# Optimization experiments

Hardware: AMD Instinct MI355X
Metric: run time of the kernel (lower is better)

## Reference

```python
import jax, jax.numpy as jnp
import numpy as np

B, C, H, W = 16, 256, 32, 32
NH, DH = 16, 16          # n_heads, n_head_channels; NH*DH == C
STRIDE, KK = 2, 9        # offset conv stride / kernel (stage_idx=0)
Hk, Wk = 16, 16          # offset map size = H/stride
NS = Hk * Wk             # n_sample
EPS_LN, EPS_BN = 1e-5, 1e-5


def conv1x1(x, w, b=None):
    # x: [B,Ci,H,W], w: [Co,Ci]
    y = jnp.einsum('bihw,oi->bohw', x, w)
    if b is not None:
        y = y + b[None, :, None, None]
    return y


def dwconv(x, w, b):
    # depthwise conv, w: [C,1,KK,KK]
    y = jax.lax.conv_general_dilated(
        x, w, (STRIDE, STRIDE), [(KK // 2, KK // 2)] * 2,
        dimension_numbers=('NCHW', 'OIHW', 'NCHW'),
        feature_group_count=x.shape[1])
    return y + b[None, :, None, None]


def ln_channels(x, g, b):
    # LayerNormProxy: layer-norm over channel dim of NCHW
    m = jnp.mean(x, axis=1, keepdims=True)
    v = jnp.mean((x - m) ** 2, axis=1, keepdims=True)
    return (x - m) / jnp.sqrt(v + EPS_LN) * g[None, :, None, None] + b[None, :, None, None]


def ref_points(hk, wk, b):
    # normalized (y, x) reference grid in [-1, 1], matching _get_ref_points
    ry = (jnp.arange(hk, dtype=jnp.float32) + 0.5) / hk * 2.0 - 1.0
    rx = (jnp.arange(wk, dtype=jnp.float32) + 0.5) / wk * 2.0 - 1.0
    ref = jnp.stack(jnp.meshgrid(ry, rx, indexing='ij'), axis=-1)  # [hk,wk,2] (y,x)
    return jnp.broadcast_to(ref[None], (b, hk, wk, 2))


def grid_sample_bilinear(img, grid):
    # img: [B,C,H,W]; grid: [B,Hg,Wg,2] in (x,y) order, [-1,1], align_corners=True,
    # zeros padding (matches torch F.grid_sample defaults).
    Bi, Ci, Hi, Wi = img.shape
    gx = (grid[..., 0] + 1.0) * 0.5 * (Wi - 1)
    gy = (grid[..., 1] + 1.0) * 0.5 * (Hi - 1)
    x0 = jnp.floor(gx); y0 = jnp.floor(gy)
    x1 = x0 + 1.0;      y1 = y0 + 1.0
    wx1 = gx - x0; wx0 = 1.0 - wx1
    wy1 = gy - y0; wy0 = 1.0 - wy1
    imgf = img.reshape(Bi, Ci, Hi * Wi)

    def gather(yi, xi):
        valid = (yi >= 0) & (yi < Hi) & (xi >= 0) & (xi < Wi)
        idx = (jnp.clip(yi, 0, Hi - 1) * Wi + jnp.clip(xi, 0, Wi - 1)).astype(jnp.int32)
        v = jnp.take_along_axis(imgf, idx.reshape(Bi, 1, -1), axis=2)  # [B,C,Hg*Wg]
        return v * valid.reshape(Bi, 1, -1).astype(img.dtype)

    out = (gather(y0, x0) * (wy0 * wx0).reshape(Bi, 1, -1)
           + gather(y0, x1) * (wy0 * wx1).reshape(Bi, 1, -1)
           + gather(y1, x0) * (wy1 * wx0).reshape(Bi, 1, -1)
           + gather(y1, x1) * (wy1 * wx1).reshape(Bi, 1, -1))
    return out.reshape(Bi, Ci, grid.shape[1], grid.shape[2])


def setup_inputs() -> dict:
    key = jax.random.key(0)
    ks = jax.random.split(key, 16)
    s = 0.05
    return {
        'x':        jax.random.normal(ks[0], (B, C, H, W), jnp.float32),
        'wq':       jax.random.normal(ks[1], (C, C), jnp.float32) * s,
        'bq':       jax.random.normal(ks[2], (C,), jnp.float32) * s,
        'off_dw_w': jax.random.normal(ks[3], (C, 1, KK, KK), jnp.float32) * s,
        'off_dw_b': jax.random.normal(ks[4], (C,), jnp.float32) * s,
        'ln_g':     jnp.ones((C,), jnp.float32),
        'ln_b':     jnp.zeros((C,), jnp.float32),
        'off_pw_w': jax.random.normal(ks[5], (2, C), jnp.float32) * s,
        'wk':       jax.random.normal(ks[6], (C, C), jnp.float32) * s,
        'bk':       jax.random.normal(ks[7], (C,), jnp.float32) * s,
        'wv':       jax.random.normal(ks[8], (C, C), jnp.float32) * s,
        'bv':       jax.random.normal(ks[9], (C,), jnp.float32) * s,
        'wo':       jax.random.normal(ks[10], (C, C), jnp.float32) * s,
        'bo':       jax.random.normal(ks[11], (C,), jnp.float32) * s,
        'bn_g':     jnp.ones((C,), jnp.float32),
        'bn_b':     jnp.zeros((C,), jnp.float32),
        'bn_m':     jax.random.normal(ks[12], (C,), jnp.float32) * s,
        'bn_v':     jax.random.uniform(ks[13], (C,), jnp.float32) + 0.5,
    }


def reference(x, wq, bq, off_dw_w, off_dw_b, ln_g, ln_b, off_pw_w,
              wk, bk, wv, bv, wo, bo, bn_g, bn_b, bn_m, bn_v):
    q = conv1x1(x, wq, bq)                                 # [B,C,H,W]
    # offset branch (n_groups=1 so q_off == q)
    off = dwconv(q, off_dw_w, off_dw_b)                    # [B,C,Hk,Wk]
    off = jax.nn.gelu(ln_channels(off, ln_g, ln_b), approximate=False)
    offset = jnp.einsum('bihw,oi->bohw', off, off_pw_w)    # [B,2,Hk,Wk] (y,x)
    offset = jnp.transpose(offset, (0, 2, 3, 1))           # [B,Hk,Wk,2]
    ref = ref_points(Hk, Wk, B)
    pos = jnp.tanh(offset + ref)                           # offset_range_factor[0] < 0 branch
    # deformable sampling: grid takes (x,y)
    xs = grid_sample_bilinear(x, pos[..., ::-1])           # [B,C,Hk,Wk]
    xs = xs.reshape(B, C, 1, NS)
    k = conv1x1(xs, wk, bk).reshape(B * NH, DH, NS)
    v = conv1x1(xs, wv, bv).reshape(B * NH, DH, NS)
    qf = q.reshape(B * NH, DH, H * W)
    attn = jnp.einsum('bcm,bcn->bmn', qf, k) * (DH ** -0.5)  # [B*NH, H*W, NS]
    attn = jax.nn.softmax(attn, axis=2)
    out = jnp.einsum('bmn,bcn->bcm', attn, v).reshape(B, C, H, W)
    y = conv1x1(out, wo, bo)
    # BatchNorm2d in eval mode with running stats
    y = ((y - bn_m[None, :, None, None]) / jnp.sqrt(bn_v[None, :, None, None] + EPS_BN)
         * bn_g[None, :, None, None] + bn_b[None, :, None, None])
    return y
```

## Files before the change

kernel.cpp:

```cpp
#include <hip/hip_runtime.h>
#include <hip/hip_bf16.h>
#include <math.h>

#define BATCH 16
#define CH    256
#define HW    1024
#define NS    256
#define NH    16
#define DH    16

typedef __attribute__((ext_vector_type(8))) short short8v;
typedef __attribute__((ext_vector_type(4))) float float4v;

__device__ __forceinline__ unsigned short f2bf(float f) {
    union { float f; unsigned u; } v; v.f = f;
    unsigned r = v.u + 0x7FFFu + ((v.u >> 16) & 1u);
    return (unsigned short)(r >> 16);
}

__global__ __launch_bounds__(256) void prep_k(
    const float* __restrict__ wq, const float* __restrict__ wk,
    const float* __restrict__ wv, const float* __restrict__ wo,
    unsigned short* __restrict__ Wf,
    const float* __restrict__ x, unsigned short* __restrict__ xT)
{
    int blk = blockIdx.x;
    if (blk < 1024) {
        const float* W;
        switch (blk >> 8) {
            case 0: W = wq; break;
            case 1: W = wk; break;
            case 2: W = wv; break;
            default: W = wo; break;
        }
        int e = (blk & 255) * 256 + threadIdx.x;
        int i = e & 7, l = (e >> 3) & 63, kt = (e >> 9) & 7, ot = e >> 12;
        float v = W[(ot * 16 + (l & 15)) * 256 + kt * 32 + 8 * (l >> 4) + i];
        Wf[(blk >> 8) * 65536 + e] = f2bf(v);
    } else {
        int xb = blk - 1024;
        int b = xb >> 4, pblk = (xb >> 2) & 3, cblk = xb & 3;
        int p = pblk * 256 + threadIdx.x;
        const float* xp = x + (size_t)b * CH * HW + p;
        unsigned short* o = xT + ((size_t)b * HW + p) * CH;
        #pragma unroll
        for (int cc = 0; cc < 64; cc += 8) {
            int c0 = cblk * 64 + cc;
            short8v t;
            #pragma unroll
            for (int i = 0; i < 8; ++i) t[i] = (short)f2bf(xp[(size_t)(c0 + i) * HW]);
            *(short8v*)&o[c0] = t;
        }
    }
}

template<int P, int MODE>
__global__ __launch_bounds__(256) void gemm_k(
    const unsigned short* __restrict__ Wf, const unsigned short* __restrict__ XT,
    const float* __restrict__ bias,
    float* __restrict__ outF, unsigned short* __restrict__ outB,
    const float* __restrict__ bn_g, const float* __restrict__ bn_b,
    const float* __restrict__ bn_m, const float* __restrict__ bn_v)
{
    const int b = blockIdx.z;

    const int t = threadIdx.x, lane = t & 63, wvi = t >> 6;
    const int g = lane >> 4, col = lane & 15;
    const int o0 = blockIdx.x * 64;
    const int p0 = blockIdx.y * 128 + wvi * 32;
    const unsigned short* xb = XT + ((size_t)b * P + p0) * CH;

    float4v acc[4][2];
    #pragma unroll
    for (int mi = 0; mi < 4; ++mi)
        #pragma unroll
        for (int ni = 0; ni < 2; ++ni) {
            float4v z = {0.f, 0.f, 0.f, 0.f};
            acc[mi][ni] = z;
        }

    #pragma unroll
    for (int kt = 0; kt < 8; ++kt) {
        short8v af[4], bf[2];
        #pragma unroll
        for (int mi = 0; mi < 4; ++mi)
            af[mi] = *(const short8v*)&Wf[(((((o0 >> 4) + mi) * 8) + kt) * 64 + lane) * 8];
        #pragma unroll
        for (int ni = 0; ni < 2; ++ni)
            bf[ni] = *(const short8v*)&xb[(size_t)(ni * 16 + col) * CH + kt * 32 + 8 * g];
        #pragma unroll
        for (int mi = 0; mi < 4; ++mi)
            #pragma unroll
            for (int ni = 0; ni < 2; ++ni)
                acc[mi][ni] = __builtin_amdgcn_mfma_f32_16x16x32_bf16(
                    af[mi], bf[ni], acc[mi][ni], 0, 0, 0);
    }

    #pragma unroll
    for (int mi = 0; mi < 4; ++mi) {
        const int ob = o0 + mi * 16 + 4 * g;
        float bs[4];
        #pragma unroll
        for (int ii = 0; ii < 4; ++ii) bs[ii] = bias[ob + ii];

        if (MODE == 2) {
            float sc[4], sh[4];
            #pragma unroll
            for (int ii = 0; ii < 4; ++ii) {
                int o = ob + ii;
                float s = bn_g[o] * rsqrtf(bn_v[o] + 1e-5f);
                sc[ii] = s;
                sh[ii] = bn_b[o] - bn_m[o] * s + bs[ii] * s;
            }
            #pragma unroll
            for (int ni = 0; ni < 2; ++ni) {
                int p = p0 + ni * 16 + col;
                #pragma unroll
                for (int ii = 0; ii < 4; ++ii)
                    outF[((size_t)(b * CH + ob + ii)) * P + p] =
                        acc[mi][ni][ii] * sc[ii] + sh[ii];
            }
        } else {
            #pragma unroll
            for (int ni = 0; ni < 2; ++ni) {
                int p = p0 + ni * 16 + col;
                float v0 = acc[mi][ni][0] + bs[0];
                float v1 = acc[mi][ni][1] + bs[1];
                float v2 = acc[mi][ni][2] + bs[2];
                float v3 = acc[mi][ni][3] + bs[3];
                outF[((size_t)(b * CH + ob + 0)) * P + p] = v0;
                outF[((size_t)(b * CH + ob + 1)) * P + p] = v1;
                outF[((size_t)(b * CH + ob + 2)) * P + p] = v2;
                outF[((size_t)(b * CH + ob + 3)) * P + p] = v3;
                uint2 w;
                w.x = (unsigned)f2bf(v0) | ((unsigned)f2bf(v1) << 16);
                w.y = (unsigned)f2bf(v2) | ((unsigned)f2bf(v3) << 16);
                *(uint2*)&outB[((size_t)(b * P + p)) * CH + ob] = w;
            }
        }
    }
}

__global__ __launch_bounds__(256) void dwconv_k(
    const float* __restrict__ q, const float* __restrict__ w,
    const float* __restrict__ bias, float* __restrict__ off)
{
    int bc = blockIdx.x;
    int c  = bc & (CH - 1);
    __shared__ float plane[HW];
    __shared__ float kw[81];
    int t = threadIdx.x;
    const float* qp = q + (size_t)bc * HW;
    #pragma unroll
    for (int j = t; j < HW; j += 256) plane[j] = qp[j];
    if (t < 81) kw[t] = w[c * 81 + t];
    __syncthreads();
    int hk = t >> 4, wk = t & 15;
    float s = bias[c];
    int yb = hk * 2 - 4, xb = wk * 2 - 4;
    #pragma unroll
    for (int dy = 0; dy < 9; ++dy) {
        int yy = yb + dy;
        if ((unsigned)yy < 32u) {
            #pragma unroll
            for (int dx = 0; dx < 9; ++dx) {
                int xx = xb + dx;
                if ((unsigned)xx < 32u) s += kw[dy * 9 + dx] * plane[yy * 32 + xx];
            }
        }
    }
    off[(size_t)bc * NS + t] = s;
}

__device__ inline void block_reduce2(float& a, float& b, int t, float* sbuf)
{
    #pragma unroll
    for (int o = 32; o > 0; o >>= 1) {
        a += __shfl_down(a, o);
        b += __shfl_down(b, o);
    }
    int w = t >> 6;
    if ((t & 63) == 0) { sbuf[w * 2] = a; sbuf[w * 2 + 1] = b; }
    __syncthreads();
    a = sbuf[0] + sbuf[2] + sbuf[4] + sbuf[6];
    b = sbuf[1] + sbuf[3] + sbuf[5] + sbuf[7];
    __syncthreads();
}

__global__ __launch_bounds__(256) void lngs_k(
    const float* __restrict__ off, const float* __restrict__ ln_g,
    const float* __restrict__ ln_b, const float* __restrict__ pw,
    const float* __restrict__ x, unsigned short* __restrict__ xsT)
{
    __shared__ float sbuf[8];
    int bs = blockIdx.x;
    int b = bs >> 8, s = bs & 255;
    int c = threadIdx.x;
    float v = off[((size_t)(b * CH + c)) * NS + s];
    float a = v, q2 = v * v;
    block_reduce2(a, q2, c, sbuf);
    float mean = a * (1.0f / 256.0f);
    float var  = q2 * (1.0f / 256.0f) - mean * mean;
    float xn = (v - mean) * rsqrtf(var + 1e-5f) * ln_g[c] + ln_b[c];
    float g = 0.5f * xn * (1.0f + erff(xn * 0.70710678118654752f));
    float d0 = g * pw[c];
    float d1 = g * pw[CH + c];
    block_reduce2(d0, d1, c, sbuf);

    int hk = s >> 4, wk = s & 15;
    float ry = ((hk + 0.5f) / 16.0f) * 2.0f - 1.0f;
    float rx = ((wk + 0.5f) / 16.0f) * 2.0f - 1.0f;
    float py = tanhf(d0 + ry);
    float px = tanhf(d1 + rx);

    float gx = (px + 1.0f) * 0.5f * 31.0f;
    float gy = (py + 1.0f) * 0.5f * 31.0f;
    float x0f = floorf(gx), y0f = floorf(gy);
    int ix = (int)x0f, iy = (int)y0f;
    float wx1 = gx - x0f, wx0 = 1.0f - wx1;
    float wy1 = gy - y0f, wy0 = 1.0f - wy1;
    const float* img = x + ((size_t)b * CH + c) * HW;
    float v00 = ((unsigned)iy < 32u && (unsigned)ix < 32u) ? img[iy * 32 + ix] : 0.0f;
    float v01 = ((unsigned)iy < 32u && (unsigned)(ix + 1) < 32u) ? img[iy * 32 + ix + 1] : 0.0f;
    float v10 = ((unsigned)(iy + 1) < 32u && (unsigned)ix < 32u) ? img[(iy + 1) * 32 + ix] : 0.0f;
    float v11 = ((unsigned)(iy + 1) < 32u && (unsigned)(ix + 1) < 32u) ? img[(iy + 1) * 32 + ix + 1] : 0.0f;
    float vv = wy0 * wx0 * v00 + wy0 * wx1 * v01 + wy1 * wx0 * v10 + wy1 * wx1 * v11;
    xsT[(size_t)bs * CH + c] = f2bf(vv);
}

__global__ __launch_bounds__(256) void attn_fused_k(
    const unsigned short* __restrict__ qT, const unsigned short* __restrict__ xsT,
    const unsigned short* __restrict__ Wf,
    const float* __restrict__ bk, const float* __restrict__ bv,
    unsigned short* __restrict__ aoT)
{
    const int bh   = blockIdx.x >> 2;
    const int mseg = blockIdx.x & 3;
    const int b = bh >> 4, h = bh & 15;

    __shared__ short Kp[16 * 64 * 8];
    __shared__ short Vp[8 * 64 * 8];
    __shared__ short Ps[4][16 * 32];

    const int tid  = threadIdx.x;
    const int lane = tid & 63;
    const int wvi  = tid >> 6;
    const int col  = lane & 15;
    const int g    = lane >> 4;

    {
        const unsigned short* WfK = Wf + 1 * 65536 + h * 4096;
        const unsigned short* WfV = Wf + 2 * 65536 + h * 4096;
        float bk4[4];
        #pragma unroll
        for (int j = 0; j < 4; ++j) bk4[j] = bk[h * 16 + 4 * g + j];
        const float bvv = bv[h * 16 + col];

        #pragma unroll
        for (int tt = 0; tt < 4; ++tt) {
            const int t  = wvi * 4 + tt;
            const int n0 = t * 16;
            float4v accK = {0.f, 0.f, 0.f, 0.f};
            float4v accV = {0.f, 0.f, 0.f, 0.f};
            #pragma unroll
            for (int kt = 0; kt < 8; ++kt) {
                short8v xsf = *(const short8v*)&xsT[((size_t)(b * NS + n0 + col)) * CH + kt * 32 + 8 * g];
                short8v wkf = *(const short8v*)&WfK[(kt * 64 + lane) * 8];
                short8v wvf = *(const short8v*)&WfV[(kt * 64 + lane) * 8];
                accK = __builtin_amdgcn_mfma_f32_16x16x32_bf16(wkf, xsf, accK, 0, 0, 0);
                accV = __builtin_amdgcn_mfma_f32_16x16x32_bf16(xsf, wvf, accV, 0, 0, 0);
            }
            uint2 wrk;
            wrk.x = (unsigned)f2bf(accK[0] + bk4[0]) | ((unsigned)f2bf(accK[1] + bk4[1]) << 16);
            wrk.y = (unsigned)f2bf(accK[2] + bk4[2]) | ((unsigned)f2bf(accK[3] + bk4[3]) << 16);
            *(uint2*)&Kp[(t * 64 + (g >> 1) * 16 + col) * 8 + 4 * (g & 1)] = wrk;
            uint2 wrv;
            wrv.x = (unsigned)f2bf(accV[0] + bvv) | ((unsigned)f2bf(accV[1] + bvv) << 16);
            wrv.y = (unsigned)f2bf(accV[2] + bvv) | ((unsigned)f2bf(accV[3] + bvv) << 16);
            *(uint2*)&Vp[((t >> 1) * 64 + col + 16 * ((2 * t + (g >> 1)) & 3)) * 8 + 4 * (g & 1)] = wrv;
        }
        short8v z = {0, 0, 0, 0, 0, 0, 0, 0};
        #pragma unroll
        for (int e = tid; e < 512; e += 256) {
            int t = e >> 5, l = e & 31;
            *(short8v*)&Kp[(t * 64 + 32 + l) * 8] = z;
        }
    }
    __syncthreads();

    const unsigned short* Qb = qT + (size_t)b * HW * CH + h * 16;
    unsigned short*       Ob = aoT + (size_t)b * HW * CH + h * 16;
    char* pbase = (char*)Ps[wvi];

    for (int mt = 0; mt < 4; ++mt) {
        const int m0 = mseg * 256 + wvi * 64 + mt * 16;

        short8v qf = {0, 0, 0, 0, 0, 0, 0, 0};
        if (g < 2)
            qf = *(const short8v*)&Qb[(size_t)(m0 + col) * CH + 8 * g];

        float4v p[16];
        #pragma unroll
        for (int t = 0; t < 16; ++t) {
            short8v kf = *(const short8v*)&Kp[(t * 64 + lane) * 8];
            float4v z = {0.f, 0.f, 0.f, 0.f};
            p[t] = __builtin_amdgcn_mfma_f32_16x16x32_bf16(kf, qf, z, 0, 0, 0);
        }

        float mx = -1e30f;
        #pragma unroll
        for (int t = 0; t < 16; ++t)
            mx = fmaxf(mx, fmaxf(fmaxf(p[t][0], p[t][1]), fmaxf(p[t][2], p[t][3])));
        mx = fmaxf(mx, __shfl_xor(mx, 16));
        mx = fmaxf(mx, __shfl_xor(mx, 32));
        float sum = 0.f;
        #pragma unroll
        for (int t = 0; t < 16; ++t) {
            #pragma unroll
            for (int i = 0; i < 4; ++i) {
                float e = __expf((p[t][i] - mx) * 0.25f);
                p[t][i] = e;
                sum += e;
            }
        }
        sum += __shfl_xor(sum, 16);
        sum += __shfl_xor(sum, 32);
        const float inv = 1.0f / sum;

        float4v acc = {0.f, 0.f, 0.f, 0.f};
        #pragma unroll
        for (int c = 0; c < 8; ++c) {
            #pragma unroll
            for (int pp = 0; pp < 2; ++pp) {
                float4v pv = p[2 * c + pp];
                uint2 wr;
                wr.x = (unsigned)f2bf(pv[0]) | ((unsigned)f2bf(pv[1]) << 16);
                wr.y = (unsigned)f2bf(pv[2]) | ((unsigned)f2bf(pv[3]) << 16);
                *(uint2*)(pbase + ((col * 64 + (16 * pp + 4 * g) * 2) ^ ((col & 7) << 4))) = wr;
            }
            short8v pf = *(const short8v*)(pbase + ((col * 64 + 16 * g) ^ ((col & 7) << 4)));
            short8v vf = *(const short8v*)&Vp[(c * 64 + lane) * 8];
            acc = __builtin_amdgcn_mfma_f32_16x16x32_bf16(vf, pf, acc, 0, 0, 0);
        }

        uint2 w;
        w.x = (unsigned)f2bf(acc[0] * inv) | ((unsigned)f2bf(acc[1] * inv) << 16);
        w.y = (unsigned)f2bf(acc[2] * inv) | ((unsigned)f2bf(acc[3] * inv) << 16);
        *(uint2*)&Ob[(size_t)(m0 + col) * CH + 4 * g] = w;
    }
}

extern "C" void kernel_launch(void* const* d_in, const int* in_sizes, int n_in,
                              void* d_out, int out_size, void* d_ws, size_t ws_size,
                              hipStream_t stream)
{
    const float* x        = (const float*)d_in[0];
    const float* wq       = (const float*)d_in[1];
    const float* bq       = (const float*)d_in[2];
    const float* off_dw_w = (const float*)d_in[3];
    const float* off_dw_b = (const float*)d_in[4];
    const float* ln_g     = (const float*)d_in[5];
    const float* ln_b     = (const float*)d_in[6];
    const float* off_pw_w = (const float*)d_in[7];
    const float* wk       = (const float*)d_in[8];
    const float* bk       = (const float*)d_in[9];
    const float* wv       = (const float*)d_in[10];
    const float* bv       = (const float*)d_in[11];
    const float* wo       = (const float*)d_in[12];
    const float* bo       = (const float*)d_in[13];
    const float* bn_g     = (const float*)d_in[14];
    const float* bn_b     = (const float*)d_in[15];
    const float* bn_m     = (const float*)d_in[16];
    const float* bn_v     = (const float*)d_in[17];

    float* ws  = (float*)d_ws;
    float* q   = ws;
    float* off = q + 4194304;
    unsigned short* us  = (unsigned short*)(off + 1048576);
    unsigned short* Wf  = us;
    unsigned short* xT  = Wf  + 262144;
    unsigned short* qT  = xT  + 4194304;
    unsigned short* xsT = qT  + 4194304;
    unsigned short* aoT = xsT + 1048576;

    prep_k<<<1280, 256, 0, stream>>>(wq, wk, wv, wo, Wf, x, xT);
    gemm_k<HW, 0><<<dim3(4, 8, BATCH), 256, 0, stream>>>(
        Wf, xT, bq, q, qT, nullptr, nullptr, nullptr, nullptr);
    dwconv_k<<<BATCH * CH, 256, 0, stream>>>(q, off_dw_w, off_dw_b, off);
    lngs_k<<<BATCH * NS, 256, 0, stream>>>(off, ln_g, ln_b, off_pw_w, x, xsT);
    attn_fused_k<<<BATCH * NH * 4, 256, 0, stream>>>(qT, xsT, Wf, bk, bv, aoT);
    gemm_k<HW, 2><<<dim3(4, 8, BATCH), 256, 0, stream>>>(
        Wf + 3 * 65536, aoT, bo, (float*)d_out, nullptr,
        bn_g, bn_b, bn_m, bn_v);
}
```

Before: 121.9 us.

## Use one 1024-thread block per head to compute K/V once

The attention kernel now runs one 1024-thread block per (batch, head) instead of four 256-thread blocks. Each of the 16 waves projects one 16-sample K/V tile, so K/V are computed once per head rather than four times. K is stored compactly, with a single zero row shared by the upper lanes in place of zero padding. The 1/sqrt(dh) scale is folded into the bf16 copy of q, and the fp32 q stays unscaled for the offset path. The change also uses the built-in bf16 conversion and tree reductions for the softmax max and sum, at the cost of fewer, larger blocks (256 total), which may reduce occupancy.

```diff
diff --git a/kernel.cpp b/kernel.cpp
--- a/kernel.cpp
+++ b/kernel.cpp
@@ -13,9 +13,10 @@
 typedef __attribute__((ext_vector_type(4))) float float4v;
 
 __device__ __forceinline__ unsigned short f2bf(float f) {
-    union { float f; unsigned u; } v; v.f = f;
-    unsigned r = v.u + 0x7FFFu + ((v.u >> 16) & 1u);
-    return (unsigned short)(r >> 16);
+    return __builtin_bit_cast(unsigned short, __float2bfloat16(f));
+}
+__device__ __forceinline__ unsigned pack2(float lo, float hi) {
+    return (unsigned)f2bf(lo) | ((unsigned)f2bf(hi) << 16);
 }
 
 __global__ __launch_bounds__(256) void prep_k(
@@ -133,8 +134,8 @@
                 outF[((size_t)(b * CH + ob + 2)) * P + p] = v2;
                 outF[((size_t)(b * CH + ob + 3)) * P + p] = v3;
                 uint2 w;
-                w.x = (unsigned)f2bf(v0) | ((unsigned)f2bf(v1) << 16);
-                w.y = (unsigned)f2bf(v2) | ((unsigned)f2bf(v3) << 16);
+                w.x = pack2(v0 * 0.25f, v1 * 0.25f);
+                w.y = pack2(v2 * 0.25f, v3 * 0.25f);
                 *(uint2*)&outB[((size_t)(b * P + p)) * CH + ob] = w;
             }
         }
@@ -228,19 +229,18 @@
     xsT[(size_t)bs * CH + c] = f2bf(vv);
 }
 
-__global__ __launch_bounds__(256) void attn_fused_k(
+__global__ __launch_bounds__(1024) void attn_fused_k(
     const unsigned short* __restrict__ qT, const unsigned short* __restrict__ xsT,
     const unsigned short* __restrict__ Wf,
     const float* __restrict__ bk, const float* __restrict__ bv,
     unsigned short* __restrict__ aoT)
 {
-    const int bh   = blockIdx.x >> 2;
-    const int mseg = blockIdx.x & 3;
+    const int bh = blockIdx.x;
     const int b = bh >> 4, h = bh & 15;
 
-    __shared__ short Kp[16 * 64 * 8];
+    __shared__ short Kp[16 * 32 * 8 + 8];
     __shared__ short Vp[8 * 64 * 8];
-    __shared__ short Ps[4][16 * 32];
+    __shared__ short Ps[16][16 * 32];
 
     const int tid  = threadIdx.x;
     const int lane = tid & 63;
@@ -256,44 +256,41 @@
         for (int j = 0; j < 4; ++j) bk4[j] = bk[h * 16 + 4 * g + j];
         const float bvv = bv[h * 16 + col];
 
-        #pragma unroll
-        for (int tt = 0; tt < 4; ++tt) {
-            const int t  = wvi * 4 + tt;
-            const int n0 = t * 16;
-            float4v accK = {0.f, 0.f, 0.f, 0.f};
-            float4v accV = {0.f, 0.f, 0.f, 0.f};
-            #pragma unroll
-            for (int kt = 0; kt < 8; ++kt) {
-                short8v xsf = *(const short8v*)&xsT[((size_t)(b * NS + n0 + col)) * CH + kt * 32 + 8 * g];
-                short8v wkf = *(const short8v*)&WfK[(kt * 64 + lane) * 8];
-                short8v wvf = *(const short8v*)&WfV[(kt * 64 + lane) * 8];
-                accK = __builtin_amdgcn_mfma_f32_16x16x32_bf16(wkf, xsf, accK, 0, 0, 0);
-                accV = __builtin_amdgcn_mfma_f32_16x16x32_bf16(xsf, wvf, accV, 0, 0, 0);
-            }
-            uint2 wrk;
-            wrk.x = (unsigned)f2bf(accK[0] + bk4[0]) | ((unsigned)f2bf(accK[1] + bk4[1]) << 16);
-            wrk.y = (unsigned)f2bf(accK[2] + bk4[2]) | ((unsigned)f2bf(accK[3] + bk4[3]) << 16);
-            *(uint2*)&Kp[(t * 64 + (g >> 1) * 16 + col) * 8 + 4 * (g & 1)] = wrk;
-            uint2 wrv;
-            wrv.x = (unsigned)f2bf(accV[0] + bvv) | ((unsigned)f2bf(accV[1] + bvv) << 16);
-            wrv.y = (unsigned)f2bf(accV[2] + bvv) | ((unsigned)f2bf(accV[3] + bvv) << 16);
-            *(uint2*)&Vp[((t >> 1) * 64 + col + 16 * ((2 * t + (g >> 1)) & 3)) * 8 + 4 * (g & 1)] = wrv;
-        }
+        const int t  = wvi;
+        const int n0 = t * 16;
+        float4v accK = {0.f, 0.f, 0.f, 0.f};
+        float4v accV = {0.f, 0.f, 0.f, 0.f};
+        #pragma unroll
+        for (int kt = 0; kt < 8; ++kt) {
+            short8v xsf = *(const short8v*)&xsT[((size_t)(b * NS + n0 + col)) * CH + kt * 32 + 8 * g];
+            short8v wkf = *(const short8v*)&WfK[(kt * 64 + lane) * 8];
+            short8v wvf = *(const short8v*)&WfV[(kt * 64 + lane) * 8];
+            accK = __builtin_amdgcn_mfma_f32_16x16x32_bf16(wkf, xsf, accK, 0, 0, 0);
+            accV = __builtin_amdgcn_mfma_f32_16x16x32_bf16(xsf, wvf, accV, 0, 0, 0);
+        }
+        uint2 wrk;
+        wrk.x = pack2(accK[0] + bk4[0], accK[1] + bk4[1]);
+        wrk.y = pack2(accK[2] + bk4[2], accK[3] + bk4[3]);
+        *(uint2*)&Kp[(t * 32 + (g >> 1) * 16 + col) * 8 + 4 * (g & 1)] = wrk;
+        uint2 wrv;
+        wrv.x = pack2(accV[0] + bvv, accV[1] + bvv);
+        wrv.y = pack2(accV[2] + bvv, accV[3] + bvv);
+        *(uint2*)&Vp[((t >> 1) * 64 + col + 16 * ((2 * t + (g >> 1)) & 3)) * 8 + 4 * (g & 1)] = wrv;
+    }
+    if (tid == 0) {
         short8v z = {0, 0, 0, 0, 0, 0, 0, 0};
-        #pragma unroll
-        for (int e = tid; e < 512; e += 256) {
-            int t = e >> 5, l = e & 31;
-            *(short8v*)&Kp[(t * 64 + 32 + l) * 8] = z;
-        }
+        *(short8v*)&Kp[16 * 32 * 8] = z;
     }
     __syncthreads();
 
     const unsigned short* Qb = qT + (size_t)b * HW * CH + h * 16;
     unsigned short*       Ob = aoT + (size_t)b * HW * CH + h * 16;
     char* pbase = (char*)Ps[wvi];
+    const char* kbase = (const char*)Kp + ((lane < 32) ? lane * 16 : 16 * 32 * 16);
+    const int   kstep = (lane < 32) ? 512 : 0;
 
     for (int mt = 0; mt < 4; ++mt) {
-        const int m0 = mseg * 256 + wvi * 64 + mt * 16;
+        const int m0 = wvi * 64 + mt * 16;
 
         short8v qf = {0, 0, 0, 0, 0, 0, 0, 0};
         if (g < 2)
@@ -302,27 +299,35 @@
         float4v p[16];
         #pragma unroll
         for (int t = 0; t < 16; ++t) {
-            short8v kf = *(const short8v*)&Kp[(t * 64 + lane) * 8];
+            short8v kf = *(const short8v*)(kbase + t * kstep);
             float4v z = {0.f, 0.f, 0.f, 0.f};
             p[t] = __builtin_amdgcn_mfma_f32_16x16x32_bf16(kf, qf, z, 0, 0, 0);
         }
 
-        float mx = -1e30f;
+        float mx4[16];
         #pragma unroll
         for (int t = 0; t < 16; ++t)
-            mx = fmaxf(mx, fmaxf(fmaxf(p[t][0], p[t][1]), fmaxf(p[t][2], p[t][3])));
+            mx4[t] = fmaxf(fmaxf(p[t][0], p[t][1]), fmaxf(p[t][2], p[t][3]));
+        #pragma unroll
+        for (int o = 8; o >= 1; o >>= 1)
+            #pragma unroll
+            for (int i = 0; i < 8; ++i)
+                if (i < o) mx4[i] = fmaxf(mx4[i], mx4[i + o]);
+        float mx = mx4[0];
         mx = fmaxf(mx, __shfl_xor(mx, 16));
         mx = fmaxf(mx, __shfl_xor(mx, 32));
-        float sum = 0.f;
+
+        float s4[4] = {0.f, 0.f, 0.f, 0.f};
         #pragma unroll
         for (int t = 0; t < 16; ++t) {
             #pragma unroll
             for (int i = 0; i < 4; ++i) {
-                float e = __expf((p[t][i] - mx) * 0.25f);
+                float e = __expf(p[t][i] - mx);
                 p[t][i] = e;
-                sum += e;
-            }
-        }
+                s4[i] += e;
+            }
+        }
+        float sum = (s4[0] + s4[1]) + (s4[2] + s4[3]);
         sum += __shfl_xor(sum, 16);
         sum += __shfl_xor(sum, 32);
         const float inv = 1.0f / sum;
@@ -334,8 +339,8 @@
             for (int pp = 0; pp < 2; ++pp) {
                 float4v pv = p[2 * c + pp];
                 uint2 wr;
-                wr.x = (unsigned)f2bf(pv[0]) | ((unsigned)f2bf(pv[1]) << 16);
-                wr.y = (unsigned)f2bf(pv[2]) | ((unsigned)f2bf(pv[3]) << 16);
+                wr.x = pack2(pv[0], pv[1]);
+                wr.y = pack2(pv[2], pv[3]);
                 *(uint2*)(pbase + ((col * 64 + (16 * pp + 4 * g) * 2) ^ ((col & 7) << 4))) = wr;
             }
             short8v pf = *(const short8v*)(pbase + ((col * 64 + 16 * g) ^ ((col & 7) << 4)));
@@ -344,8 +349,8 @@
         }
 
         uint2 w;
-        w.x = (unsigned)f2bf(acc[0] * inv) | ((unsigned)f2bf(acc[1] * inv) << 16);
-        w.y = (unsigned)f2bf(acc[2] * inv) | ((unsigned)f2bf(acc[3] * inv) << 16);
+        w.x = pack2(acc[0] * inv, acc[1] * inv);
+        w.y = pack2(acc[2] * inv, acc[3] * inv);
         *(uint2*)&Ob[(size_t)(m0 + col) * CH + 4 * g] = w;
     }
 }
@@ -388,7 +393,7 @@
         Wf, xT, bq, q, qT, nullptr, nullptr, nullptr, nullptr);
     dwconv_k<<<BATCH * CH, 256, 0, stream>>>(q, off_dw_w, off_dw_b, off);
     lngs_k<<<BATCH * NS, 256, 0, stream>>>(off, ln_g, ln_b, off_pw_w, x, xsT);
-    attn_fused_k<<<BATCH * NH * 4, 256, 0, stream>>>(qT, xsT, Wf, bk, bv, aoT);
+    attn_fused_k<<<BATCH * NH, 1024, 0, stream>>>(qT, xsT, Wf, bk, bv, aoT);
     gemm_k<HW, 2><<<dim3(4, 8, BATCH), 256, 0, stream>>>(
         Wf + 3 * 65536, aoT, bo, (float*)d_out, nullptr,
         bn_g, bn_b, bn_m, bn_v);
```

New measurement: 150.0 us. 1.23x slower.
